# Kernel tuning notes

Hardware: AMD Instinct MI355X
Metric: run time of the kernel (lower is better)

## Reference

```python
import jax, jax.numpy as jnp
import numpy as np

N_USERS, N_ITEMS, K, D, B = 100000, 50000, 20, 64, 16384
CAT = 2 * D  # 128


def setup_inputs() -> dict:
    key = jax.random.key(0)
    ks = jax.random.split(key, 14)
    user_idx_tensor = jax.random.randint(ks[0], (N_USERS, K), 0, N_USERS)
    user_scr_tensor = jax.random.uniform(ks[1], (N_USERS, K), dtype=jnp.float32)
    item_idx_tensor = jax.random.randint(ks[2], (N_ITEMS, K), 0, N_ITEMS)
    item_scr_tensor = jax.random.uniform(ks[3], (N_ITEMS, K), dtype=jnp.float32)
    user_emb_table = jax.random.normal(ks[4], (N_USERS, D), dtype=jnp.float32) * 0.02
    item_emb_table = jax.random.normal(ks[5], (N_ITEMS, D), dtype=jnp.float32) * 0.02
    # InterLin: Linear(128->64), Linear(64->32), Linear(32->1); stored as (in,out)
    w1 = jax.random.normal(ks[6], (CAT, CAT // 2), dtype=jnp.float32) * (1.0 / np.sqrt(CAT))
    b1 = jnp.zeros((CAT // 2,), dtype=jnp.float32)
    w2 = jax.random.normal(ks[7], (CAT // 2, CAT // 4), dtype=jnp.float32) * (1.0 / np.sqrt(CAT // 2))
    b2 = jnp.zeros((CAT // 4,), dtype=jnp.float32)
    w3 = jax.random.normal(ks[8], (CAT // 4, 1), dtype=jnp.float32) * (1.0 / np.sqrt(CAT // 4))
    b3 = jnp.zeros((1,), dtype=jnp.float32)
    user_idxs = jax.random.randint(ks[9], (B,), 0, N_USERS)
    item_idxs = jax.random.randint(ks[10], (B,), 0, N_ITEMS)
    return {
        "user_idxs": user_idxs, "item_idxs": item_idxs,
        "user_idx_tensor": user_idx_tensor, "user_scr_tensor": user_scr_tensor,
        "item_idx_tensor": item_idx_tensor, "item_scr_tensor": item_scr_tensor,
        "user_emb_table": user_emb_table, "item_emb_table": item_emb_table,
        "w1": w1, "b1": b1, "w2": w2, "b2": b2, "w3": w3, "b3": b3,
    }


def reference(user_idxs, item_idxs, user_idx_tensor, user_scr_tensor,
              item_idx_tensor, item_scr_tensor, user_emb_table, item_emb_table,
              w1, b1, w2, b2, w3, b3):
    # user side
    user_neighs = user_idx_tensor[user_idxs]            # [B,K]
    neigh_emb = user_emb_table[user_neighs]             # [B,K,D]
    neigh_score = user_scr_tensor[user_neighs]          # [B,K,K]
    scored_user_emb = jnp.einsum('bkj,bjd->bkd', neigh_score, neigh_emb)
    # item side
    item_neighs = item_idx_tensor[item_idxs]            # [B,K]
    item_neigh_emb = item_emb_table[item_neighs]        # [B,K,D]
    item_neigh_scr = item_scr_tensor[item_neighs]       # [B,K,K]
    scored_item_emb = jnp.einsum('bkj,bjd->bkd', item_neigh_scr, item_neigh_emb)
    # concat + 3-layer MLP + sigmoid + mean over neighbor axis
    x = jnp.concatenate((scored_user_emb, scored_item_emb), axis=2)  # [B,K,2D]
    h = jax.nn.relu(x @ w1 + b1)
    h = jax.nn.relu(h @ w2 + b2)
    logits = h @ w3 + b3                                # [B,K,1]
    result = jax.nn.sigmoid(logits)
    return jnp.mean(result, axis=-2).squeeze()          # [B]
```

## Files before the change

### kernel.cpp

```cpp
#include <hip/hip_runtime.h>
#include <hip/hip_bf16.h>
#include <math.h>

#define KN 20
#define DD 64
#define WPB 4
#define NUSERS 100000
#define NITEMS 50000
#define NBU 1024
#define NBI 512
#define NBS 128
#define SROW 24

typedef __hip_bfloat16 bf16;
typedef __attribute__((ext_vector_type(8))) short short8;
typedef __attribute__((ext_vector_type(16))) float f32x16;

__device__ inline ushort f2bf(float f) {
    unsigned u = __builtin_bit_cast(unsigned, f);
    u += 0x7fffu + ((u >> 16) & 1u);
    return (ushort)(u >> 16);
}

__global__ __launch_bounds__(256, 4) void precompute_Y(
    const float* __restrict__ emb_u, const float* __restrict__ emb_i,
    const float* __restrict__ w1, const float* __restrict__ w2,
    const float* __restrict__ uscr, const float* __restrict__ iscr,
    bf16* __restrict__ Yu, bf16* __restrict__ Yi, ushort* __restrict__ w2b,
    ushort* __restrict__ sbu, ushort* __restrict__ sbi)
{
    __shared__ float stage[WPB][256];
    const int w    = threadIdx.x >> 6;
    const int lane = threadIdx.x & 63;

    if ((int)blockIdx.x >= NBU + NBI) {
        const int t0 = ((int)blockIdx.x - (NBU + NBI)) * 256 + (int)threadIdx.x;
        const int NCH = 3 * (NUSERS + NITEMS);
        for (int cch = t0; cch < NCH; cch += NBS * 256) {
            int r = cch / 3, part = cch - 3 * r;
            const float* src = (r < NUSERS) ? (uscr + (size_t)r * KN)
                                            : (iscr + (size_t)(r - NUSERS) * KN);
            ushort* dst = (r < NUSERS) ? (sbu + (size_t)r * SROW)
                                       : (sbi + (size_t)(r - NUSERS) * SROW);
            ushort tmp[8];
            if (part < 2) {
                float4 v0 = *(const float4*)(src + 8 * part);
                float4 v1 = *(const float4*)(src + 8 * part + 4);
                tmp[0] = f2bf(v0.x); tmp[1] = f2bf(v0.y);
                tmp[2] = f2bf(v0.z); tmp[3] = f2bf(v0.w);
                tmp[4] = f2bf(v1.x); tmp[5] = f2bf(v1.y);
                tmp[6] = f2bf(v1.z); tmp[7] = f2bf(v1.w);
            } else {
                float4 v0 = *(const float4*)(src + 16);
                tmp[0] = f2bf(v0.x); tmp[1] = f2bf(v0.y);
                tmp[2] = f2bf(v0.z); tmp[3] = f2bf(v0.w);
                tmp[4] = tmp[5] = tmp[6] = tmp[7] = 0;
            }
            *(short8*)(dst + 8 * part) = *(const short8*)tmp;
        }
        return;
    }

    if ((int)blockIdx.x == NBU + NBI - 1) {
        const int tid = threadIdx.x;
        const int t = tid >> 6, gg = (tid >> 5) & 1, o = tid & 31;
        #pragma unroll
        for (int j = 0; j < 8; ++j)
            w2b[(size_t)tid * 8 + j] = f2bf(w2[(16 * t + 8 * gg + j) * 32 + o]);
    }

    const bool isU = (int)blockIdx.x < NBU;
    const float* __restrict__ emb  = isU ? emb_u : emb_i;
    bf16* __restrict__       Y     = isU ? Yu : Yi;
    const float* __restrict__ wsrc = isU ? w1 : (w1 + 64 * DD);
    const int ngroups = (isU ? NUSERS : NITEMS) / 4;
    const int bidx    = isU ? (int)blockIdx.x : ((int)blockIdx.x - NBU);
    const int nwaves  = (isU ? NBU : NBI) * WPB;
    const int wid     = bidx * WPB + w;

    float wreg[64];
    #pragma unroll
    for (int c = 0; c < 64; ++c) wreg[c] = wsrc[c * DD + lane];

    for (int g = wid; g < ngroups; g += nwaves) {
        float4 v = *(const float4*)&emb[(size_t)g * 256 + lane * 4];
        *(float4*)&stage[w][lane * 4] = v;
        #pragma unroll
        for (int r = 0; r < 4; ++r) {
            float a0 = 0.f, a1 = 0.f, a2 = 0.f, a3 = 0.f;
            #pragma unroll
            for (int q = 0; q < 16; ++q) {
                float4 e4 = *(const float4*)&stage[w][r * 64 + q * 4];
                a0 = fmaf(e4.x, wreg[q * 4 + 0], a0);
                a1 = fmaf(e4.y, wreg[q * 4 + 1], a1);
                a2 = fmaf(e4.z, wreg[q * 4 + 2], a2);
                a3 = fmaf(e4.w, wreg[q * 4 + 3], a3);
            }
            Y[(size_t)(g * 4 + r) * DD + lane] = (bf16)((a0 + a1) + (a2 + a3));
        }
    }
}

template<bool SBF>
__global__ __launch_bounds__(256, 8) void cnn_main(
    const int* __restrict__ user_idxs, const int* __restrict__ item_idxs,
    const int* __restrict__ user_idx_tensor, const float* __restrict__ uscr_f,
    const ushort* __restrict__ uscr_b,
    const int* __restrict__ item_idx_tensor, const float* __restrict__ iscr_f,
    const ushort* __restrict__ iscr_b,
    const bf16* __restrict__ Yu, const bf16* __restrict__ Yi,
    const float* __restrict__ b1, const ushort* __restrict__ w2b,
    const float* __restrict__ b2,
    const float* __restrict__ w3, const float* __restrict__ b3,
    float* __restrict__ out, int Bn)
{
    __shared__ ushort buf[WPB][3072];

    const int w    = threadIdx.x >> 6;
    const int lane = threadIdx.x & 63;
    const int g    = lane >> 5;
    const int c    = lane & 31;
    const int b = blockIdx.x * WPB + w;
    if (b >= Bn) return;

    const int uid = user_idxs[b];
    const int iid = item_idxs[b];

    int nvu = 0, nvi = 0;
    if (lane < KN) {
        nvu = user_idx_tensor[uid * KN + lane];
        nvi = item_idx_tensor[iid * KN + lane];
    }

    #pragma unroll
    for (int side = 0; side < 2; ++side) {
        const ushort* Y = (const ushort*)(side ? Yi : Yu);
        const int nv = side ? nvi : nvu;
        #pragma unroll
        for (int i = 0; i < 3; ++i) {
            int nr = __shfl(nv, 8 * i + (lane >> 3));
            short8 v = *(const short8*)(Y + (size_t)nr * DD + (lane & 7) * 8);
            *(short8*)&buf[w][side * 1536 + i * 512 + lane * 8] = v;
        }
    }

    f32x16 acc0 = {};
    f32x16 acc1 = {};

    #pragma unroll
    for (int side = 0; side < 2; ++side) {
        const int nv = side ? nvi : nvu;
        const int n_r = __shfl(nv, c);

        short8 A0, A1;
        if (SBF) {
            const ushort* sr = (side ? iscr_b : uscr_b) + (size_t)n_r * SROW;
            A0 = *(const short8*)(sr + 8 * g);
            A1 = *(const short8*)(sr + 16);
        } else {
            const float* arow = (side ? iscr_f : uscr_f) + (size_t)n_r * KN;
            float4 a0 = *(const float4*)(arow + 8 * g);
            float4 a1 = *(const float4*)(arow + 8 * g + 4);
            A0[0] = (short)f2bf(a0.x); A0[1] = (short)f2bf(a0.y);
            A0[2] = (short)f2bf(a0.z); A0[3] = (short)f2bf(a0.w);
            A0[4] = (short)f2bf(a1.x); A0[5] = (short)f2bf(a1.y);
            A0[6] = (short)f2bf(a1.z); A0[7] = (short)f2bf(a1.w);
            float4 a2 = *(const float4*)(arow + 16);
            A1 = short8{};
            A1[0] = (short)f2bf(a2.x); A1[1] = (short)f2bf(a2.y);
            A1[2] = (short)f2bf(a2.z); A1[3] = (short)f2bf(a2.w);
        }

        const int sb0 = side * 1536;
        short8 B00, B01;
        #pragma unroll
        for (int j = 0; j < 8; ++j) {
            B00[j] = (short)buf[w][sb0 + (8 * g + j) * DD + c];
            B01[j] = (short)buf[w][sb0 + (8 * g + j) * DD + 32 + c];
        }
        acc0 = __builtin_amdgcn_mfma_f32_32x32x16_bf16(A0, B00, acc0, 0, 0, 0);
        acc1 = __builtin_amdgcn_mfma_f32_32x32x16_bf16(A0, B01, acc1, 0, 0, 0);

        short8 B10 = {}, B11 = {};
        if (g == 0) {
            #pragma unroll
            for (int j = 0; j < 4; ++j) {
                B10[j] = (short)buf[w][sb0 + (16 + j) * DD + c];
                B11[j] = (short)buf[w][sb0 + (16 + j) * DD + 32 + c];
            }
        }
        acc0 = __builtin_amdgcn_mfma_f32_32x32x16_bf16(A1, B10, acc0, 0, 0, 0);
        acc1 = __builtin_amdgcn_mfma_f32_32x32x16_bf16(A1, B11, acc1, 0, 0, 0);
    }

    const float b1v0 = b1[c];
    const float b1v1 = b1[32 + c];
    #pragma unroll
    for (int r = 0; r < 12; ++r) {
        const int row = (r & 3) + 8 * (r >> 2) + 4 * g;
        if (row < KN) {
            const int ch0 = (c >> 3) ^ (row & 7);
            const int ch1 = (4 + (c >> 3)) ^ (row & 7);
            buf[w][row * DD + ch0 * 8 + (c & 7)] = f2bf(fmaxf(acc0[r] + b1v0, 0.f));
            buf[w][row * DD + ch1 * 8 + (c & 7)] = f2bf(fmaxf(acc1[r] + b1v1, 0.f));
        }
    }

    const int ar = (c < KN) ? c : 0;
    f32x16 c2 = {};
    #pragma unroll
    for (int t = 0; t < 4; ++t) {
        const int chunk = (2 * t + g) ^ (ar & 7);
        short8 A = *(const short8*)&buf[w][ar * DD + chunk * 8];
        short8 B = *(const short8*)&w2b[(size_t)(((t * 2 + g) * 32 + c)) * 8];
        c2 = __builtin_amdgcn_mfma_f32_32x32x16_bf16(A, B, c2, 0, 0, 0);
    }

    const float b2v = b2[c];
    const float w3v = w3[c];
    const float b3v = b3[0];
    float sum = 0.f;
    #pragma unroll
    for (int r = 0; r < 12; ++r) {
        float h2v = fmaxf(c2[r] + b2v, 0.f);
        float p = h2v * w3v;
        #pragma unroll
        for (int off = 16; off > 0; off >>= 1)
            p += __shfl_xor(p, off);
        float logit = p + b3v;
        if (g == 0 || r < 8)
            sum += 1.f / (1.f + __expf(-logit));
    }
    sum += __shfl_xor(sum, 32);
    if (lane == 0) out[b] = sum * (1.f / KN);
}

extern "C" void kernel_launch(void* const* d_in, const int* in_sizes, int n_in,
                              void* d_out, int out_size, void* d_ws, size_t ws_size,
                              hipStream_t stream) {
    const int*   user_idxs       = (const int*)  d_in[0];
    const int*   item_idxs       = (const int*)  d_in[1];
    const int*   user_idx_tensor = (const int*)  d_in[2];
    const float* user_scr_tensor = (const float*)d_in[3];
    const int*   item_idx_tensor = (const int*)  d_in[4];
    const float* item_scr_tensor = (const float*)d_in[5];
    const float* user_emb        = (const float*)d_in[6];
    const float* item_emb        = (const float*)d_in[7];
    const float* w1 = (const float*)d_in[8];
    const float* b1 = (const float*)d_in[9];
    const float* w2 = (const float*)d_in[10];
    const float* b2 = (const float*)d_in[11];
    const float* w3 = (const float*)d_in[12];
    const float* b3 = (const float*)d_in[13];
    float* out = (float*)d_out;

    const int Bn = in_sizes[0];

    bf16*   Yu  = (bf16*)d_ws;
    bf16*   Yi  = Yu + (size_t)NUSERS * DD;
    ushort* w2b = (ushort*)(Yi + (size_t)NITEMS * DD);
    ushort* sbu = w2b + 2048;
    ushort* sbi = sbu + (size_t)NUSERS * SROW;

    const size_t need = (size_t)(NUSERS + NITEMS) * DD * 2 + 2048 * 2
                      + (size_t)(NUSERS + NITEMS) * SROW * 2;
    const bool big = ws_size >= need;

    precompute_Y<<<NBU + NBI + (big ? NBS : 0), 256, 0, stream>>>(
        user_emb, item_emb, w1, w2, user_scr_tensor, item_scr_tensor,
        Yu, Yi, w2b, sbu, sbi);

    const int grid = (Bn + WPB - 1) / WPB;
    if (big)
        cnn_main<true><<<grid, 256, 0, stream>>>(
            user_idxs, item_idxs, user_idx_tensor, user_scr_tensor, sbu,
            item_idx_tensor, item_scr_tensor, sbi, Yu, Yi,
            b1, w2b, b2, w3, b3, out, Bn);
    else
        cnn_main<false><<<grid, 256, 0, stream>>>(
            user_idxs, item_idxs, user_idx_tensor, user_scr_tensor, sbu,
            item_idx_tensor, item_scr_tensor, sbi, Yu, Yi,
            b1, w2b, b2, w3, b3, out, Bn);
}
```

Measured before the change: 62.62 us.

## Compute one embedding row per lane in precompute_Y with register accumulators

```diff
diff --git a/kernel.cpp b/kernel.cpp
--- a/kernel.cpp
+++ b/kernel.cpp
@@ -7,8 +7,10 @@
 #define WPB 4
 #define NUSERS 100000
 #define NITEMS 50000
-#define NBU 1024
-#define NBI 512
+#define UGROUPS 1563
+#define IGROUPS 782
+#define TGROUPS (UGROUPS + IGROUPS)
+#define NBY 587
 #define NBS 128
 #define SROW 24
 
@@ -29,12 +31,12 @@
     bf16* __restrict__ Yu, bf16* __restrict__ Yi, ushort* __restrict__ w2b,
     ushort* __restrict__ sbu, ushort* __restrict__ sbi)
 {
-    __shared__ float stage[WPB][256];
     const int w    = threadIdx.x >> 6;
     const int lane = threadIdx.x & 63;
-
-    if ((int)blockIdx.x >= NBU + NBI) {
-        const int t0 = ((int)blockIdx.x - (NBU + NBI)) * 256 + (int)threadIdx.x;
+    const int bid  = (int)blockIdx.x;
+
+    if (bid >= NBY) {
+        const int t0 = (bid - NBY) * 256 + (int)threadIdx.x;
         const int NCH = 3 * (NUSERS + NITEMS);
         for (int cch = t0; cch < NCH; cch += NBS * 256) {
             int r = cch / 3, part = cch - 3 * r;
@@ -61,7 +63,7 @@
         return;
     }
 
-    if ((int)blockIdx.x == NBU + NBI - 1) {
+    if (bid == NBY - 1) {
         const int tid = threadIdx.x;
         const int t = tid >> 6, gg = (tid >> 5) & 1, o = tid & 31;
         #pragma unroll
@@ -69,35 +71,40 @@
             w2b[(size_t)tid * 8 + j] = f2bf(w2[(16 * t + 8 * gg + j) * 32 + o]);
     }
 
-    const bool isU = (int)blockIdx.x < NBU;
+    const int g = bid * WPB + w;
+    if (g >= TGROUPS) return;
+    const bool isU = g < UGROUPS;
     const float* __restrict__ emb  = isU ? emb_u : emb_i;
-    bf16* __restrict__       Y     = isU ? Yu : Yi;
+    bf16* __restrict__        Y    = isU ? Yu : Yi;
     const float* __restrict__ wsrc = isU ? w1 : (w1 + 64 * DD);
-    const int ngroups = (isU ? NUSERS : NITEMS) / 4;
-    const int bidx    = isU ? (int)blockIdx.x : ((int)blockIdx.x - NBU);
-    const int nwaves  = (isU ? NBU : NBI) * WPB;
-    const int wid     = bidx * WPB + w;
-
-    float wreg[64];
-    #pragma unroll
-    for (int c = 0; c < 64; ++c) wreg[c] = wsrc[c * DD + lane];
-
-    for (int g = wid; g < ngroups; g += nwaves) {
-        float4 v = *(const float4*)&emb[(size_t)g * 256 + lane * 4];
-        *(float4*)&stage[w][lane * 4] = v;
-        #pragma unroll
-        for (int r = 0; r < 4; ++r) {
-            float a0 = 0.f, a1 = 0.f, a2 = 0.f, a3 = 0.f;
+    const int nrows = isU ? NUSERS : NITEMS;
+    int row = (isU ? g : (g - UGROUPS)) * 64 + lane;
+    if (row >= nrows) row = nrows - 1;
+
+    const float* __restrict__ er = emb + (size_t)row * DD;
+    float acc[64];
+    #pragma unroll
+    for (int o = 0; o < 64; ++o) acc[o] = 0.f;
+
+    for (int cq = 0; cq < 16; ++cq) {
+        float4 e4 = *(const float4*)(er + cq * 4);
+        #pragma unroll
+        for (int cc = 0; cc < 4; ++cc) {
+            const float ev = (cc == 0) ? e4.x : (cc == 1) ? e4.y : (cc == 2) ? e4.z : e4.w;
+            const float* __restrict__ wr = wsrc + (cq * 4 + cc) * DD;
             #pragma unroll
-            for (int q = 0; q < 16; ++q) {
-                float4 e4 = *(const float4*)&stage[w][r * 64 + q * 4];
-                a0 = fmaf(e4.x, wreg[q * 4 + 0], a0);
-                a1 = fmaf(e4.y, wreg[q * 4 + 1], a1);
-                a2 = fmaf(e4.z, wreg[q * 4 + 2], a2);
-                a3 = fmaf(e4.w, wreg[q * 4 + 3], a3);
-            }
-            Y[(size_t)(g * 4 + r) * DD + lane] = (bf16)((a0 + a1) + (a2 + a3));
-        }
+            for (int o = 0; o < 64; ++o)
+                acc[o] = fmaf(ev, wr[o], acc[o]);
+        }
+    }
+
+    ushort* yrow = (ushort*)Y + (size_t)row * DD;
+    #pragma unroll
+    for (int q = 0; q < 8; ++q) {
+        ushort tmp[8];
+        #pragma unroll
+        for (int j = 0; j < 8; ++j) tmp[j] = f2bf(acc[q * 8 + j]);
+        *(short8*)(yrow + q * 8) = *(const short8*)tmp;
     }
 }
 
@@ -266,7 +273,7 @@
                       + (size_t)(NUSERS + NITEMS) * SROW * 2;
     const bool big = ws_size >= need;
 
-    precompute_Y<<<NBU + NBI + (big ? NBS : 0), 256, 0, stream>>>(
+    precompute_Y<<<NBY + (big ? NBS : 0), 256, 0, stream>>>(
         user_emb, item_emb, w1, w2, user_scr_tensor, item_scr_tensor,
         Yu, Yi, w2b, sbu, sbi);
 
```

New measurement: 136.5 us. 118% more time.
